# Kernel optimization log

Measured on AMD Instinct MI355X. Metric: run time of the kernel, lower is better.

The kernel has to match this reference:

```python
import jax, jax.numpy as jnp
import numpy as np

SIZE = 4096
DOWN = SIZE // 16  # reduction_factor = 16 -> 256
N_TASKS = 16
BATCH = 2048
INIT_STD = 0.01


def setup_inputs() -> dict:
    key = jax.random.key(0)
    k_x, k_t, k_wd, k_wu = jax.random.split(key, 4)
    x = jax.random.normal(k_x, (BATCH, SIZE), dtype=jnp.float32)
    task_id = jax.random.randint(k_t, (BATCH,), 0, N_TASKS)
    # Stacked per-task adapter params (init: normal(std=0.01) weights, zero bias)
    Wd = jax.random.normal(k_wd, (N_TASKS, SIZE, DOWN), dtype=jnp.float32) * INIT_STD
    bd = jnp.zeros((N_TASKS, DOWN), dtype=jnp.float32)
    Wu = jax.random.normal(k_wu, (N_TASKS, DOWN, SIZE), dtype=jnp.float32) * INIT_STD
    bu = jnp.zeros((N_TASKS, SIZE), dtype=jnp.float32)
    return {"x": x, "task_id": task_id, "Wd": Wd, "bd": bd, "Wu": Wu, "bu": bu}


def reference(x, task_id, Wd, bd, Wu, bu):
    # Down-projection for all tasks, then select each sample's routed task.
    # [B, T, DOWN] is small (B*T*256), cheaper than gathering [B, SIZE, DOWN] weights.
    down_all = jnp.einsum('bd,tdh->bth', x, Wd) + bd[None]
    down = jnp.take_along_axis(down_all, task_id[:, None, None], axis=1)[:, 0]  # [B, DOWN]
    act = jax.nn.silu(down)
    # Up-projection for all tasks, select routed task. [B, T, SIZE]
    up_all = jnp.einsum('bh,thd->btd', act, Wu) + bu[None]
    up = jnp.take_along_axis(up_all, task_id[:, None, None], axis=1)[:, 0]  # [B, SIZE]
    return x + up  # residual=True (default)
```

## Files before the change

### kernel.cpp

```cpp
#include <hip/hip_runtime.h>

#define BATCH 2048
#define SIZE 4096
#define DOWN 256
#define NTASK 16
#define KC 8
#define KCHUNK (SIZE / KC)

typedef _Float16 half8 __attribute__((ext_vector_type(8)));
typedef float floatx4 __attribute__((ext_vector_type(4)));

__device__ __forceinline__ int imin(int a, int b) { return a < b ? a : b; }
__device__ __forceinline__ int uswz(int n) { return n ^ ((n >> 3) & 7); }

__global__ __launch_bounds__(256) void sort_kernel(const int* __restrict__ task_id,
                                                   int* __restrict__ taskOff,
                                                   int* __restrict__ sortedIdx,
                                                   int* __restrict__ taskOfPos) {
    __shared__ int cnt[NTASK];
    __shared__ int base[NTASK + 1];
    __shared__ int cur[NTASK];
    int tid = threadIdx.x;
    if (tid < NTASK) cnt[tid] = 0;
    __syncthreads();
    for (int i = tid; i < BATCH; i += 256) atomicAdd(&cnt[task_id[i]], 1);
    __syncthreads();
    if (tid == 0) {
        int s = 0;
        for (int t = 0; t < NTASK; t++) { base[t] = s; s += cnt[t]; }
        base[NTASK] = s;
    }
    __syncthreads();
    if (tid < NTASK) { cur[tid] = base[tid]; taskOff[tid] = base[tid]; }
    if (tid == 0) taskOff[NTASK] = BATCH;
    __syncthreads();
    for (int i = tid; i < BATCH; i += 256) {
        int t = task_id[i];
        int p = atomicAdd(&cur[t], 1);
        sortedIdx[p] = i;
        taskOfPos[p] = t;
    }
}

__global__ __launch_bounds__(256, 2) void gemm1_kernel(const float* __restrict__ x,
                                                       const float* __restrict__ Wd,
                                                       const int* __restrict__ taskOff,
                                                       const int* __restrict__ sortedIdx,
                                                       _Float16* __restrict__ partial) {
    int task = blockIdx.x >> 1, z = blockIdx.x & 1, kc = blockIdx.y;
    int rowStart = taskOff[task];
    int nrows = taskOff[task + 1] - rowStart;
    if (nrows <= 0) return;

    __shared__ half8 A_lds[8][65];
    __shared__ half8 B_lds[8][256];

    int tid = threadIdx.x;
    int wave = tid >> 6, lane = tid & 63, quad = lane >> 4, l15 = lane & 15;
    int kbase0 = kc * KCHUNK;
    const float* Wdt = Wd + (size_t)task * SIZE * DOWN;

    int bswz[4];
#pragma unroll
    for (int i = 0; i < 4; i++) bswz[i] = uswz(wave * 64 + i * 16 + l15);

    for (int r0 = z * 64; r0 < nrows; r0 += 128) {
        floatx4 acc[4][4];
#pragma unroll
        for (int mi = 0; mi < 4; mi++)
#pragma unroll
            for (int ni = 0; ni < 4; ni++) acc[mi][ni] = (floatx4){0.f, 0.f, 0.f, 0.f};

        int arow = tid >> 2;
        int asrc = sortedIdx[rowStart + imin(r0 + arow, nrows - 1)];
        const float* xrow = x + (size_t)asrc * SIZE;

        for (int kb = 0; kb < KCHUNK; kb += 64) {
            int kglob = kbase0 + kb;
            floatx4 fa[2][2];
#pragma unroll
            for (int j = 0; j < 2; j++) {
                int kg = ((tid & 3) << 1) | j;
                const float* src = xrow + kglob + kg * 8;
                fa[j][0] = *(const floatx4*)(src);
                fa[j][1] = *(const floatx4*)(src + 4);
            }
            floatx4 fb[2][8];
#pragma unroll
            for (int s = 0; s < 2; s++) {
                int kg = s * 4 + wave;
                const float* src = Wdt + (size_t)(kglob + kg * 8) * DOWN + lane * 4;
#pragma unroll
                for (int j = 0; j < 8; j++) fb[s][j] = *(const floatx4*)(src + (size_t)j * DOWN);
            }
            __syncthreads();
#pragma unroll
            for (int j = 0; j < 2; j++) {
                int kg = ((tid & 3) << 1) | j;
                half8 h;
                h[0] = (_Float16)fa[j][0][0]; h[1] = (_Float16)fa[j][0][1];
                h[2] = (_Float16)fa[j][0][2]; h[3] = (_Float16)fa[j][0][3];
                h[4] = (_Float16)fa[j][1][0]; h[5] = (_Float16)fa[j][1][1];
                h[6] = (_Float16)fa[j][1][2]; h[7] = (_Float16)fa[j][1][3];
                A_lds[kg][arow] = h;
            }
#pragma unroll
            for (int s = 0; s < 2; s++) {
                int kg = s * 4 + wave;
#pragma unroll
                for (int i = 0; i < 4; i++) {
                    half8 h;
#pragma unroll
                    for (int j = 0; j < 8; j++) h[j] = (_Float16)fb[s][j][i];
                    B_lds[kg][uswz(lane * 4 + i)] = h;
                }
            }
            __syncthreads();
#pragma unroll
            for (int ks = 0; ks < 2; ks++) {
                int kg = ks * 4 + quad;
                half8 a[4], b[4];
#pragma unroll
                for (int i = 0; i < 4; i++) a[i] = A_lds[kg][i * 16 + l15];
#pragma unroll
                for (int i = 0; i < 4; i++) b[i] = B_lds[kg][bswz[i]];
#pragma unroll
                for (int mi = 0; mi < 4; mi++)
#pragma unroll
                    for (int ni = 0; ni < 4; ni++)
                        acc[mi][ni] = __builtin_amdgcn_mfma_f32_16x16x32_f16(
                            a[mi], b[ni], acc[mi][ni], 0, 0, 0);
            }
        }
#pragma unroll
        for (int mi = 0; mi < 4; mi++) {
#pragma unroll
            for (int reg = 0; reg < 4; reg++) {
                int r = r0 + mi * 16 + quad * 4 + reg;
                if (r < nrows) {
                    size_t rowoff = ((size_t)kc * BATCH + (rowStart + r)) * DOWN;
#pragma unroll
                    for (int ni = 0; ni < 4; ni++) {
                        int h = wave * 64 + ni * 16 + l15;
                        partial[rowoff + h] = (_Float16)acc[mi][ni][reg];
                    }
                }
            }
        }
    }
}

__global__ __launch_bounds__(256) void silu_kernel(const _Float16* __restrict__ partial,
                                                   const float* __restrict__ bd,
                                                   const int* __restrict__ taskOfPos,
                                                   _Float16* __restrict__ act) {
    int idx = blockIdx.x * 256 + threadIdx.x;
    int s = idx >> 5;
    int h = (idx & 31) * 8;
    int t = taskOfPos[s];
    floatx4 b0 = *(const floatx4*)(bd + t * DOWN + h);
    floatx4 b1 = *(const floatx4*)(bd + t * DOWN + h + 4);
    float v[8];
    v[0] = b0[0]; v[1] = b0[1]; v[2] = b0[2]; v[3] = b0[3];
    v[4] = b1[0]; v[5] = b1[1]; v[6] = b1[2]; v[7] = b1[3];
#pragma unroll
    for (int kc = 0; kc < KC; kc++) {
        half8 p = *(const half8*)(partial + ((size_t)kc * BATCH + s) * DOWN + h);
#pragma unroll
        for (int j = 0; j < 8; j++) v[j] += (float)p[j];
    }
    half8 o;
#pragma unroll
    for (int j = 0; j < 8; j++) {
        float sv = v[j] / (1.0f + __expf(-v[j]));
        o[j] = (_Float16)sv;
    }
    *(half8*)(act + (size_t)s * DOWN + h) = o;
}

__global__ __launch_bounds__(256, 2) void gemm2_kernel(const _Float16* __restrict__ act,
                                                       const float* __restrict__ Wu,
                                                       const float* __restrict__ bu,
                                                       const float* __restrict__ x,
                                                       const int* __restrict__ taskOff,
                                                       const int* __restrict__ sortedIdx,
                                                       float* __restrict__ out) {
    int nt = blockIdx.x, task = blockIdx.y;
    int rowStart = taskOff[task];
    int nrows = taskOff[task + 1] - rowStart;
    if (nrows <= 0) return;

    __shared__ half8 A_lds[8][129];
    __shared__ half8 B_lds[8][128];

    int tid = threadIdx.x;
    int wave = tid >> 6, lane = tid & 63, quad = lane >> 4, l15 = lane & 15;
    int wm = wave >> 1, wn = wave & 1;
    int ncol0 = nt * 128;
    const float* Wut = Wu + (size_t)task * DOWN * SIZE;

    int bswz[4];
#pragma unroll
    for (int i = 0; i < 4; i++) bswz[i] = uswz(wn * 64 + i * 16 + l15);
    int kgB = tid >> 5, nfB = tid & 31;

    for (int r0 = 0; r0 < nrows; r0 += 128) {
        floatx4 acc[4][4];
#pragma unroll
        for (int mi = 0; mi < 4; mi++)
#pragma unroll
            for (int ni = 0; ni < 4; ni++) acc[mi][ni] = (floatx4){0.f, 0.f, 0.f, 0.f};

        int arow = tid >> 1;
        int s_a = rowStart + imin(r0 + arow, nrows - 1);
        const _Float16* actrow = act + (size_t)s_a * DOWN;

        for (int kb = 0; kb < DOWN; kb += 64) {
            half8 ha[4];
#pragma unroll
            for (int j = 0; j < 4; j++) {
                int kg = ((tid & 1) << 2) | j;
                ha[j] = *(const half8*)(actrow + kb + kg * 8);
            }
            floatx4 fb[8];
            const float* src = Wut + (size_t)(kb + kgB * 8) * SIZE + ncol0 + nfB * 4;
#pragma unroll
            for (int j = 0; j < 8; j++) fb[j] = *(const floatx4*)(src + (size_t)j * SIZE);
            __syncthreads();
#pragma unroll
            for (int j = 0; j < 4; j++) {
                int kg = ((tid & 1) << 2) | j;
                A_lds[kg][arow] = ha[j];
            }
#pragma unroll
            for (int i = 0; i < 4; i++) {
                half8 h;
#pragma unroll
                for (int j = 0; j < 8; j++) h[j] = (_Float16)fb[j][i];
                B_lds[kgB][uswz(nfB * 4 + i)] = h;
            }
            __syncthreads();
#pragma unroll
            for (int ks = 0; ks < 2; ks++) {
                int kg = ks * 4 + quad;
                half8 a[4], b[4];
#pragma unroll
                for (int i = 0; i < 4; i++) a[i] = A_lds[kg][wm * 64 + i * 16 + l15];
#pragma unroll
                for (int i = 0; i < 4; i++) b[i] = B_lds[kg][bswz[i]];
#pragma unroll
                for (int mi = 0; mi < 4; mi++)
#pragma unroll
                    for (int ni = 0; ni < 4; ni++)
                        acc[mi][ni] = __builtin_amdgcn_mfma_f32_16x16x32_f16(
                            a[mi], b[ni], acc[mi][ni], 0, 0, 0);
            }
        }
#pragma unroll
        for (int mi = 0; mi < 4; mi++) {
#pragma unroll
            for (int reg = 0; reg < 4; reg++) {
                int r = r0 + wm * 64 + mi * 16 + quad * 4 + reg;
                if (r < nrows) {
                    int b = sortedIdx[rowStart + r];
                    const float* xr = x + (size_t)b * SIZE;
                    float* outr = out + (size_t)b * SIZE;
#pragma unroll
                    for (int ni = 0; ni < 4; ni++) {
                        int n = ncol0 + wn * 64 + ni * 16 + l15;
                        __builtin_nontemporal_store(
                            acc[mi][ni][reg] + bu[task * SIZE + n] + xr[n], outr + n);
                    }
                }
            }
        }
    }
}

extern "C" void kernel_launch(void* const* d_in, const int* in_sizes, int n_in,
                              void* d_out, int out_size, void* d_ws, size_t ws_size,
                              hipStream_t stream) {
    const float* x       = (const float*)d_in[0];
    const int*   task_id = (const int*)d_in[1];
    const float* Wd      = (const float*)d_in[2];
    const float* bd      = (const float*)d_in[3];
    const float* Wu      = (const float*)d_in[4];
    const float* bu      = (const float*)d_in[5];
    float* out = (float*)d_out;

    _Float16* partial = (_Float16*)d_out;
    _Float16* act     = (_Float16*)d_ws;
    int* taskOff   = (int*)(act + (size_t)BATCH * DOWN);
    int* sortedIdx = taskOff + 32;
    int* taskOfPos = sortedIdx + BATCH;

    sort_kernel<<<1, 256, 0, stream>>>(task_id, taskOff, sortedIdx, taskOfPos);
    gemm1_kernel<<<dim3(NTASK * 2, KC), 256, 0, stream>>>(x, Wd, taskOff, sortedIdx, partial);
    silu_kernel<<<(BATCH * DOWN / 8) / 256, 256, 0, stream>>>(partial, bd, taskOfPos, act);
    gemm2_kernel<<<dim3(SIZE / 128, NTASK), 256, 0, stream>>>(act, Wu, bu, x, taskOff,
                                                              sortedIdx, out);
}
```

Baseline: 242.4 us.

## Fuse sort, GEMMs and SiLU into one cooperative kernel with grid syncs

Replaces four separate kernel launches with a single cooperative kernel of 512 blocks that runs the sort, down-projection, SiLU and up-projection phases separated by grid-wide barriers, with a fallback to the old launch sequence if the cooperative launch fails. The split-K factor for the down-projection doubles so its grid matches the 512 blocks, and shared memory moves into one common buffer. This removes launch gaps and per-kernel tail effects. In exchange it adds grid-sync cost, needs all 512 blocks resident at once, writes twice as much partial data, and runs the sort on a single block while the rest wait.

```diff
diff --git a/kernel.cpp b/kernel.cpp
--- a/kernel.cpp
+++ b/kernel.cpp
@@ -1,11 +1,14 @@
 #include <hip/hip_runtime.h>
+#include <hip/hip_cooperative_groups.h>
 
 #define BATCH 2048
 #define SIZE 4096
 #define DOWN 256
 #define NTASK 16
-#define KC 8
+#define KC 16
 #define KCHUNK (SIZE / KC)
+
+namespace cg = cooperative_groups;
 
 typedef _Float16 half8 __attribute__((ext_vector_type(8)));
 typedef float floatx4 __attribute__((ext_vector_type(4)));
@@ -13,13 +16,15 @@
 __device__ __forceinline__ int imin(int a, int b) { return a < b ? a : b; }
 __device__ __forceinline__ int uswz(int n) { return n ^ ((n >> 3) & 7); }
 
-__global__ __launch_bounds__(256) void sort_kernel(const int* __restrict__ task_id,
-                                                   int* __restrict__ taskOff,
-                                                   int* __restrict__ sortedIdx,
-                                                   int* __restrict__ taskOfPos) {
-    __shared__ int cnt[NTASK];
-    __shared__ int base[NTASK + 1];
-    __shared__ int cur[NTASK];
+#define SMEM_BYTES 41088
+
+
+__device__ void sort_body(char* smem, const int* __restrict__ task_id,
+                          int* __restrict__ taskOff, int* __restrict__ sortedIdx,
+                          int* __restrict__ taskOfPos) {
+    int* cnt = (int*)smem;
+    int* base = cnt + NTASK;
+    int* cur = base + NTASK + 1;
     int tid = threadIdx.x;
     if (tid < NTASK) cnt[tid] = 0;
     __syncthreads();
@@ -42,18 +47,17 @@
     }
 }
 
-__global__ __launch_bounds__(256, 2) void gemm1_kernel(const float* __restrict__ x,
-                                                       const float* __restrict__ Wd,
-                                                       const int* __restrict__ taskOff,
-                                                       const int* __restrict__ sortedIdx,
-                                                       _Float16* __restrict__ partial) {
-    int task = blockIdx.x >> 1, z = blockIdx.x & 1, kc = blockIdx.y;
+__device__ void gemm1_body(char* smem, int task, int kc, int z,
+                           const float* __restrict__ x, const float* __restrict__ Wd,
+                           const int* __restrict__ taskOff,
+                           const int* __restrict__ sortedIdx,
+                           _Float16* __restrict__ partial) {
     int rowStart = taskOff[task];
     int nrows = taskOff[task + 1] - rowStart;
     if (nrows <= 0) return;
 
-    __shared__ half8 A_lds[8][65];
-    __shared__ half8 B_lds[8][256];
+    half8(*A_lds)[65] = (half8(*)[65])smem;
+    half8(*B_lds)[256] = (half8(*)[256])(smem + 8 * 65 * 16);
 
     int tid = threadIdx.x;
     int wave = tid >> 6, lane = tid & 63, quad = lane >> 4, l15 = lane & 15;
@@ -150,11 +154,10 @@
     }
 }
 
-__global__ __launch_bounds__(256) void silu_kernel(const _Float16* __restrict__ partial,
-                                                   const float* __restrict__ bd,
-                                                   const int* __restrict__ taskOfPos,
-                                                   _Float16* __restrict__ act) {
-    int idx = blockIdx.x * 256 + threadIdx.x;
+__device__ void silu_body(int idx, const _Float16* __restrict__ partial,
+                          const float* __restrict__ bd,
+                          const int* __restrict__ taskOfPos,
+                          _Float16* __restrict__ act) {
     int s = idx >> 5;
     int h = (idx & 31) * 8;
     int t = taskOfPos[s];
@@ -178,6 +181,162 @@
     *(half8*)(act + (size_t)s * DOWN + h) = o;
 }
 
+__device__ void gemm2_body(char* smem, int nt, int task,
+                           const _Float16* __restrict__ act,
+                           const float* __restrict__ Wu, const float* __restrict__ bu,
+                           const float* __restrict__ x, const int* __restrict__ taskOff,
+                           const int* __restrict__ sortedIdx, float* __restrict__ out) {
+    int rowStart = taskOff[task];
+    int nrows = taskOff[task + 1] - rowStart;
+    if (nrows <= 0) return;
+
+    half8(*A_lds)[129] = (half8(*)[129])smem;
+    half8(*B_lds)[128] = (half8(*)[128])(smem + 8 * 129 * 16);
+
+    int tid = threadIdx.x;
+    int wave = tid >> 6, lane = tid & 63, quad = lane >> 4, l15 = lane & 15;
+    int wm = wave >> 1, wn = wave & 1;
+    int ncol0 = nt * 128;
+    const float* Wut = Wu + (size_t)task * DOWN * SIZE;
+
+    int bswz[4];
+#pragma unroll
+    for (int i = 0; i < 4; i++) bswz[i] = uswz(wn * 64 + i * 16 + l15);
+    int kgB = tid >> 5, nfB = tid & 31;
+
+    for (int r0 = 0; r0 < nrows; r0 += 128) {
+        floatx4 acc[4][4];
+#pragma unroll
+        for (int mi = 0; mi < 4; mi++)
+#pragma unroll
+            for (int ni = 0; ni < 4; ni++) acc[mi][ni] = (floatx4){0.f, 0.f, 0.f, 0.f};
+
+        int arow = tid >> 1;
+        int s_a = rowStart + imin(r0 + arow, nrows - 1);
+        const _Float16* actrow = act + (size_t)s_a * DOWN;
+
+        for (int kb = 0; kb < DOWN; kb += 64) {
+            half8 ha[4];
+#pragma unroll
+            for (int j = 0; j < 4; j++) {
+                int kg = ((tid & 1) << 2) | j;
+                ha[j] = *(const half8*)(actrow + kb + kg * 8);
+            }
+            floatx4 fb[8];
+            const float* src = Wut + (size_t)(kb + kgB * 8) * SIZE + ncol0 + nfB * 4;
+#pragma unroll
+            for (int j = 0; j < 8; j++) fb[j] = *(const floatx4*)(src + (size_t)j * SIZE);
+            __syncthreads();
+#pragma unroll
+            for (int j = 0; j < 4; j++) {
+                int kg = ((tid & 1) << 2) | j;
+                A_lds[kg][arow] = ha[j];
+            }
+#pragma unroll
+            for (int i = 0; i < 4; i++) {
+                half8 h;
+#pragma unroll
+                for (int j = 0; j < 8; j++) h[j] = (_Float16)fb[j][i];
+                B_lds[kgB][uswz(nfB * 4 + i)] = h;
+            }
+            __syncthreads();
+#pragma unroll
+            for (int ks = 0; ks < 2; ks++) {
+                int kg = ks * 4 + quad;
+                half8 a[4], b[4];
+#pragma unroll
+                for (int i = 0; i < 4; i++) a[i] = A_lds[kg][wm * 64 + i * 16 + l15];
+#pragma unroll
+                for (int i = 0; i < 4; i++) b[i] = B_lds[kg][bswz[i]];
+#pragma unroll
+                for (int mi = 0; mi < 4; mi++)
+#pragma unroll
+                    for (int ni = 0; ni < 4; ni++)
+                        acc[mi][ni] = __builtin_amdgcn_mfma_f32_16x16x32_f16(
+                            a[mi], b[ni], acc[mi][ni], 0, 0, 0);
+            }
+        }
+#pragma unroll
+        for (int mi = 0; mi < 4; mi++) {
+#pragma unroll
+            for (int reg = 0; reg < 4; reg++) {
+                int r = r0 + wm * 64 + mi * 16 + quad * 4 + reg;
+                if (r < nrows) {
+                    int b = sortedIdx[rowStart + r];
+                    const float* xr = x + (size_t)b * SIZE;
+                    float* outr = out + (size_t)b * SIZE;
+#pragma unroll
+                    for (int ni = 0; ni < 4; ni++) {
+                        int n = ncol0 + wn * 64 + ni * 16 + l15;
+                        __builtin_nontemporal_store(
+                            acc[mi][ni][reg] + bu[task * SIZE + n] + xr[n], outr + n);
+                    }
+                }
+            }
+        }
+    }
+}
+
+__global__ __launch_bounds__(256, 2) void fused_kernel(
+    const float* __restrict__ x, const int* __restrict__ task_id,
+    const float* __restrict__ Wd, const float* __restrict__ bd,
+    const float* __restrict__ Wu, const float* __restrict__ bu,
+    float* __restrict__ out, _Float16* __restrict__ partial,
+    _Float16* __restrict__ act, int* __restrict__ taskOff,
+    int* __restrict__ sortedIdx, int* __restrict__ taskOfPos) {
+    __shared__ __align__(16) char smem[SMEM_BYTES];
+    cg::grid_group grid = cg::this_grid();
+    int bid = blockIdx.x;
+
+    if (bid == 0) sort_body(smem, task_id, taskOff, sortedIdx, taskOfPos);
+    __threadfence();
+    grid.sync();
+
+    {
+        int task = bid >> 5, kc = (bid >> 1) & 15, z = bid & 1;
+        gemm1_body(smem, task, kc, z, x, Wd, taskOff, sortedIdx, partial);
+    }
+    __threadfence();
+    grid.sync();
+
+    {
+        int idx = bid * 256 + threadIdx.x;
+        if (idx < (BATCH * DOWN / 8)) silu_body(idx, partial, bd, taskOfPos, act);
+    }
+    __threadfence();
+    grid.sync();
+
+    {
+        int nt = bid & 31, task = bid >> 5;
+        gemm2_body(smem, nt, task, act, Wu, bu, x, taskOff, sortedIdx, out);
+    }
+}
+
+__global__ __launch_bounds__(256) void sort_kernel(const int* __restrict__ task_id,
+                                                   int* __restrict__ taskOff,
+                                                   int* __restrict__ sortedIdx,
+                                                   int* __restrict__ taskOfPos) {
+    __shared__ __align__(16) char smem[256];
+    sort_body(smem, task_id, taskOff, sortedIdx, taskOfPos);
+}
+
+__global__ __launch_bounds__(256, 2) void gemm1_kernel(const float* __restrict__ x,
+                                                       const float* __restrict__ Wd,
+                                                       const int* __restrict__ taskOff,
+                                                       const int* __restrict__ sortedIdx,
+                                                       _Float16* __restrict__ partial) {
+    __shared__ __align__(16) char smem[SMEM_BYTES];
+    gemm1_body(smem, blockIdx.x >> 1, blockIdx.y, blockIdx.x & 1, x, Wd, taskOff,
+               sortedIdx, partial);
+}
+
+__global__ __launch_bounds__(256) void silu_kernel(const _Float16* __restrict__ partial,
+                                                   const float* __restrict__ bd,
+                                                   const int* __restrict__ taskOfPos,
+                                                   _Float16* __restrict__ act) {
+    silu_body(blockIdx.x * 256 + threadIdx.x, partial, bd, taskOfPos, act);
+}
+
 __global__ __launch_bounds__(256, 2) void gemm2_kernel(const _Float16* __restrict__ act,
                                                        const float* __restrict__ Wu,
                                                        const float* __restrict__ bu,
@@ -185,96 +344,8 @@
                                                        const int* __restrict__ taskOff,
                                                        const int* __restrict__ sortedIdx,
                                                        float* __restrict__ out) {
-    int nt = blockIdx.x, task = blockIdx.y;
-    int rowStart = taskOff[task];
-    int nrows = taskOff[task + 1] - rowStart;
-    if (nrows <= 0) return;
-
-    __shared__ half8 A_lds[8][129];
-    __shared__ half8 B_lds[8][128];
-
-    int tid = threadIdx.x;
-    int wave = tid >> 6, lane = tid & 63, quad = lane >> 4, l15 = lane & 15;
-    int wm = wave >> 1, wn = wave & 1;
-    int ncol0 = nt * 128;
-    const float* Wut = Wu + (size_t)task * DOWN * SIZE;
-
-    int bswz[4];
-#pragma unroll
-    for (int i = 0; i < 4; i++) bswz[i] = uswz(wn * 64 + i * 16 + l15);
-    int kgB = tid >> 5, nfB = tid & 31;
-
-    for (int r0 = 0; r0 < nrows; r0 += 128) {
-        floatx4 acc[4][4];
-#pragma unroll
-        for (int mi = 0; mi < 4; mi++)
-#pragma unroll
-            for (int ni = 0; ni < 4; ni++) acc[mi][ni] = (floatx4){0.f, 0.f, 0.f, 0.f};
-
-        int arow = tid >> 1;
-        int s_a = rowStart + imin(r0 + arow, nrows - 1);
-        const _Float16* actrow = act + (size_t)s_a * DOWN;
-
-        for (int kb = 0; kb < DOWN; kb += 64) {
-            half8 ha[4];
-#pragma unroll
-            for (int j = 0; j < 4; j++) {
-                int kg = ((tid & 1) << 2) | j;
-                ha[j] = *(const half8*)(actrow + kb + kg * 8);
-            }
-            floatx4 fb[8];
-            const float* src = Wut + (size_t)(kb + kgB * 8) * SIZE + ncol0 + nfB * 4;
-#pragma unroll
-            for (int j = 0; j < 8; j++) fb[j] = *(const floatx4*)(src + (size_t)j * SIZE);
-            __syncthreads();
-#pragma unroll
-            for (int j = 0; j < 4; j++) {
-                int kg = ((tid & 1) << 2) | j;
-                A_lds[kg][arow] = ha[j];
-            }
-#pragma unroll
-            for (int i = 0; i < 4; i++) {
-                half8 h;
-#pragma unroll
-                for (int j = 0; j < 8; j++) h[j] = (_Float16)fb[j][i];
-                B_lds[kgB][uswz(nfB * 4 + i)] = h;
-            }
-            __syncthreads();
-#pragma unroll
-            for (int ks = 0; ks < 2; ks++) {
-                int kg = ks * 4 + quad;
-                half8 a[4], b[4];
-#pragma unroll
-                for (int i = 0; i < 4; i++) a[i] = A_lds[kg][wm * 64 + i * 16 + l15];
-#pragma unroll
-                for (int i = 0; i < 4; i++) b[i] = B_lds[kg][bswz[i]];
-#pragma unroll
-                for (int mi = 0; mi < 4; mi++)
-#pragma unroll
-                    for (int ni = 0; ni < 4; ni++)
-                        acc[mi][ni] = __builtin_amdgcn_mfma_f32_16x16x32_f16(
-                            a[mi], b[ni], acc[mi][ni], 0, 0, 0);
-            }
-        }
-#pragma unroll
-        for (int mi = 0; mi < 4; mi++) {
-#pragma unroll
-            for (int reg = 0; reg < 4; reg++) {
-                int r = r0 + wm * 64 + mi * 16 + quad * 4 + reg;
-                if (r < nrows) {
-                    int b = sortedIdx[rowStart + r];
-                    const float* xr = x + (size_t)b * SIZE;
-                    float* outr = out + (size_t)b * SIZE;
-#pragma unroll
-                    for (int ni = 0; ni < 4; ni++) {
-                        int n = ncol0 + wn * 64 + ni * 16 + l15;
-                        __builtin_nontemporal_store(
-                            acc[mi][ni][reg] + bu[task * SIZE + n] + xr[n], outr + n);
-                    }
-                }
-            }
-        }
-    }
+    __shared__ __align__(16) char smem[SMEM_BYTES];
+    gemm2_body(smem, blockIdx.x, blockIdx.y, act, Wu, bu, x, taskOff, sortedIdx, out);
 }
 
 extern "C" void kernel_launch(void* const* d_in, const int* in_sizes, int n_in,
@@ -294,9 +365,19 @@
     int* sortedIdx = taskOff + 32;
     int* taskOfPos = sortedIdx + BATCH;
 
-    sort_kernel<<<1, 256, 0, stream>>>(task_id, taskOff, sortedIdx, taskOfPos);
-    gemm1_kernel<<<dim3(NTASK * 2, KC), 256, 0, stream>>>(x, Wd, taskOff, sortedIdx, partial);
-    silu_kernel<<<(BATCH * DOWN / 8) / 256, 256, 0, stream>>>(partial, bd, taskOfPos, act);
-    gemm2_kernel<<<dim3(SIZE / 128, NTASK), 256, 0, stream>>>(act, Wu, bu, x, taskOff,
-                                                              sortedIdx, out);
-}
+    void* args[] = {(void*)&x,   (void*)&task_id, (void*)&Wd,        (void*)&bd,
+                    (void*)&Wu,  (void*)&bu,      (void*)&out,       (void*)&partial,
+                    (void*)&act, (void*)&taskOff, (void*)&sortedIdx, (void*)&taskOfPos};
+    hipError_t err = hipLaunchCooperativeKernel((const void*)fused_kernel, dim3(512),
+                                                dim3(256), args, 0, stream);
+    if (err != hipSuccess) {
+        sort_kernel<<<1, 256, 0, stream>>>(task_id, taskOff, sortedIdx, taskOfPos);
+        gemm1_kernel<<<dim3(NTASK * 2, KC), 256, 0, stream>>>(x, Wd, taskOff,
+                                                              sortedIdx, partial);
+        silu_kernel<<<(BATCH * DOWN / 8) / 256, 256, 0, stream>>>(partial, bd,
+                                                                  taskOfPos, act);
+        gemm2_kernel<<<dim3(SIZE / 128, NTASK), 256, 0, stream>>>(act, Wu, bu, x,
+                                                                  taskOff, sortedIdx,
+                                                                  out);
+    }
+}
```

After: 584.3 us. 141% more time.
